# Optimization experiments

Measured on AMD Instinct MI355X. Metric: run time of the kernel, lower is better.

## Reference

```python
import jax, jax.numpy as jnp
import numpy as np

RADIUS = 2          # DKD soft-detection radius -> 5x5 patch
KSIZE = 2 * RADIUS + 1
TEMP = 0.1          # softmax temperature
TOP_K = 2048        # top_k>0 branch: static keypoint count
NMS_R = 3           # simple_nms radius hardcoded in detect_keypoints


def _maxpool(x, r):
    k = 2 * r + 1
    return jax.lax.reduce_window(
        x, -jnp.inf, jax.lax.max,
        (1, 1, k, k), (1, 1, 1, 1),
        ((0, 0), (0, 0), (r, r), (r, r)))


def _maxpool_split(x, r):
    # faithful to max_pool_parallel: pools top/bottom halves independently
    half = x.shape[2] // 2
    return jnp.concatenate([_maxpool(x[:, :, :half], r),
                            _maxpool(x[:, :, half:], r)], axis=2)


def _simple_nms(s, r):
    mm = s == _maxpool_split(s, r)
    for _ in range(2):
        sm = _maxpool_split(mm.astype(s.dtype), r) > 0
        ss = jnp.where(sm, 0.0, s)
        nm = ss == _maxpool_split(ss, r)
        mm = mm | (nm & ~sm)
    return jnp.where(mm, s, 0.0)


def _bilinear(img, xy):
    # grid_sample, mode='bilinear', align_corners=True
    # img: [B,C,H,W], xy: [B,K,2] in [-1,1] (x,y) -> [B,K,C]
    b, c, h, w = img.shape
    imgt = jnp.transpose(img, (0, 2, 3, 1))  # [B,H,W,C]
    x = (xy[..., 0] + 1.0) * 0.5 * (w - 1)
    y = (xy[..., 1] + 1.0) * 0.5 * (h - 1)
    x0 = jnp.floor(x); y0 = jnp.floor(y)
    wx = (x - x0)[..., None]; wy = (y - y0)[..., None]
    x0i = jnp.clip(x0, 0, w - 1).astype(jnp.int32)
    x1i = jnp.clip(x0 + 1, 0, w - 1).astype(jnp.int32)
    y0i = jnp.clip(y0, 0, h - 1).astype(jnp.int32)
    y1i = jnp.clip(y0 + 1, 0, h - 1).astype(jnp.int32)
    bi = jnp.arange(b)[:, None]
    g = lambda yi, xi: imgt[bi, yi, xi]
    return (g(y0i, x0i) * (1 - wx) * (1 - wy) + g(y0i, x1i) * wx * (1 - wy)
            + g(y1i, x0i) * (1 - wx) * wy + g(y1i, x1i) * wx * wy)


def setup_inputs() -> dict:
    key = jax.random.key(0)
    k1, k2 = jax.random.split(key)
    scores_map = jax.random.uniform(k1, (2, 1, 512, 512), dtype=jnp.float32)
    descriptor_map = jax.random.normal(k2, (2, 128, 512, 512), dtype=jnp.float32)
    return {"scores_map": scores_map, "descriptor_map": descriptor_map}


def reference(scores_map, descriptor_map):
    b, _, h, w = scores_map.shape
    r = RADIUS
    dt = scores_map.dtype
    # --- NMS on detached scores ---
    s_ng = jax.lax.stop_gradient(scores_map)
    nms = _simple_nms(s_ng, NMS_R)
    yi = jnp.arange(h); xi = jnp.arange(w)
    border = (((yi >= r + 1) & (yi < h - r))[:, None]
              & ((xi >= r + 1) & (xi < w - r))[None, :])
    nms = nms * border
    # --- top_k keypoint selection (static shape [B,K]) ---
    _, idx = jax.lax.top_k(nms.reshape(b, -1), TOP_K)
    ky = idx // w; kx = idx % w
    # --- gather 5x5 patches (== unfold + fancy index), zero padded ---
    pad = jnp.pad(scores_map[:, 0], ((0, 0), (r, r), (r, r)))
    offs = jnp.arange(KSIZE)
    dyg, dxg = jnp.meshgrid(offs, offs, indexing='ij')
    dy = dyg.reshape(-1); dx = dxg.reshape(-1)           # [25]
    bi = jnp.arange(b)[:, None, None]
    patch = pad[bi, ky[:, :, None] + dy, kx[:, :, None] + dx]   # [B,K,25]
    # hw_grid: (dx, dy) pairs, row-major over (dy, dx) like unfold
    lin = jnp.linspace(-r, r, KSIZE).astype(dt)
    gy, gx = jnp.meshgrid(lin, lin, indexing='ij')
    hw = jnp.stack([gx.reshape(-1), gy.reshape(-1)], axis=-1)   # [25,2]
    # --- soft-argmax subpixel refinement ---
    maxv = jax.lax.stop_gradient(patch.max(-1, keepdims=True))
    xexp = jnp.exp((patch - maxv) / TEMP)
    ssum = xexp.sum(-1)
    xy_res = jnp.einsum('bkp,pc->bkc', xexp, hw) / ssum[..., None]  # [B,K,2]
    d2 = jnp.sum(((hw[None, None] - xy_res[:, :, None]) / r) ** 2, axis=-1)
    disp = (xexp * d2).sum(-1) / ssum                     # [B,K]
    kxy = jnp.stack([kx, ky], axis=-1).astype(dt) + xy_res
    kxy = kxy / jnp.array([w - 1, h - 1], dt) * 2.0 - 1.0  # [-1,1]
    # --- bilinear sampling of scores + descriptors ---
    kptscores = _bilinear(scores_map, kxy)[..., 0]        # [B,K]
    desc = _bilinear(descriptor_map, kxy)                 # [B,K,C]
    desc = desc / jnp.maximum(jnp.linalg.norm(desc, axis=-1, keepdims=True), 1e-12)
    return (kxy, desc, kptscores, disp)
```

## Files before the change

### kernel.cpp

```cpp
#include <hip/hip_runtime.h>
#include <cstdint>
#include <cstddef>

#define H 512
#define W 512
#define NPIX (H * W)
#define TOPK 2048
#define CAND_CAP 4096
#define NBATCH 2

#define RG 62
#define RS 64
#define NTOT (RG * RS)

struct Tap {
    int x0, x1, y0, y1;
    float wx, wy;
    float pad0, pad1;
};

__global__ void k_zero(unsigned int* __restrict__ hist, unsigned int* __restrict__ cnt) {
    int i = blockIdx.x * 256 + threadIdx.x;
    if (i < NBATCH * 65536) hist[i] = 0;
    if (i < 8) cnt[i] = 0;
}

__global__ __launch_bounds__(256) void k_nms_fused(
        const float* __restrict__ s, float* __restrict__ nms,
        unsigned int* __restrict__ hist) {
    __shared__ float A[NTOT];
    __shared__ float Bf[NTOT];
    __shared__ float Cf[NTOT];
    __shared__ unsigned char Mmm[NTOT];
    __shared__ unsigned char Msm[NTOT];
    __shared__ unsigned char Mt[NTOT];

    const int tid = threadIdx.x;
    const int b = blockIdx.z;
    const int gx0 = blockIdx.x * 32 - 15;
    const int gy0 = blockIdx.y * 32 - 15;
    const int h0 = (blockIdx.y < 8) ? 0 : 256;
    const int h1 = h0 + 256;
    const float* sb = s + (size_t)b * NPIX;

    for (int i = tid; i < NTOT; i += 256) {
        int x = i & 63, y = i >> 6;
        float v = -INFINITY;
        int gx = gx0 + x, gy = gy0 + y;
        if (x < RG && gx >= 0 && gx < W && gy >= h0 && gy < h1)
            v = sb[gy * W + gx];
        A[i] = v;
    }
    __syncthreads();

    for (int i = tid; i < NTOT; i += 256) {
        int x = i & 63;
        if (x >= 3 && x < 59) {
            float m = A[i - 3];
            m = fmaxf(m, A[i - 2]); m = fmaxf(m, A[i - 1]); m = fmaxf(m, A[i]);
            m = fmaxf(m, A[i + 1]); m = fmaxf(m, A[i + 2]); m = fmaxf(m, A[i + 3]);
            Cf[i] = m;
        }
    }
    __syncthreads();

    for (int i = tid; i < NTOT; i += 256) {
        int x = i & 63, y = i >> 6;
        if (x >= 3 && x < 59 && y >= 3 && y < 59) {
            float m = Cf[i - 3 * RS];
            m = fmaxf(m, Cf[i - 2 * RS]); m = fmaxf(m, Cf[i - RS]);
            m = fmaxf(m, Cf[i]);
            m = fmaxf(m, Cf[i + RS]); m = fmaxf(m, Cf[i + 2 * RS]);
            m = fmaxf(m, Cf[i + 3 * RS]);
            Mmm[i] = (A[i] == m) ? 1 : 0;
        }
    }
    __syncthreads();

    for (int it = 0; it < 2; ++it) {
        const int lo1 = 6 + 6 * it, hi1 = RG - lo1;
        const int lo0 = lo1 - 3,    hi0 = RG - lo0;
        const int lo2 = lo1 + 3,    hi2 = RG - lo2;

        for (int i = tid; i < NTOT; i += 256) {
            int x = i & 63, y = i >> 6;
            if (x >= lo1 && x < hi1 && y >= lo0 && y < hi0) {
                Mt[i] = (unsigned char)(Mmm[i - 3] | Mmm[i - 2] | Mmm[i - 1] |
                                        Mmm[i] | Mmm[i + 1] | Mmm[i + 2] | Mmm[i + 3]);
            }
        }
        __syncthreads();

        for (int i = tid; i < NTOT; i += 256) {
            int x = i & 63, y = i >> 6;
            if (x >= lo1 && x < hi1 && y >= lo1 && y < hi1) {
                unsigned char o = (unsigned char)(Mt[i - 3 * RS] | Mt[i - 2 * RS] |
                                                  Mt[i - RS] | Mt[i] | Mt[i + RS] |
                                                  Mt[i + 2 * RS] | Mt[i + 3 * RS]);
                Msm[i] = o;
                Bf[i] = o ? 0.0f : A[i];
            }
        }
        __syncthreads();

        for (int i = tid; i < NTOT; i += 256) {
            int x = i & 63, y = i >> 6;
            if (x >= lo2 && x < hi2 && y >= lo1 && y < hi1) {
                float m = Bf[i - 3];
                m = fmaxf(m, Bf[i - 2]); m = fmaxf(m, Bf[i - 1]); m = fmaxf(m, Bf[i]);
                m = fmaxf(m, Bf[i + 1]); m = fmaxf(m, Bf[i + 2]); m = fmaxf(m, Bf[i + 3]);
                Cf[i] = m;
            }
        }
        __syncthreads();

        if (it == 0) {
            for (int i = tid; i < NTOT; i += 256) {
                int x = i & 63, y = i >> 6;
                if (x >= lo2 && x < hi2 && y >= lo2 && y < hi2) {
                    float m = Cf[i - 3 * RS];
                    m = fmaxf(m, Cf[i - 2 * RS]); m = fmaxf(m, Cf[i - RS]);
                    m = fmaxf(m, Cf[i]);
                    m = fmaxf(m, Cf[i + RS]); m = fmaxf(m, Cf[i + 2 * RS]);
                    m = fmaxf(m, Cf[i + 3 * RS]);
                    int nm = (Bf[i] == m) ? 1 : 0;
                    Mmm[i] = (unsigned char)(Mmm[i] | (nm & (1 - (int)Msm[i])));
                }
            }
            __syncthreads();
        } else {
            for (int i = tid; i < NTOT; i += 256) {
                int x = i & 63, y = i >> 6;
                if (x >= 15 && x < 47 && y >= 15 && y < 47) {
                    float m = Cf[i - 3 * RS];
                    m = fmaxf(m, Cf[i - 2 * RS]); m = fmaxf(m, Cf[i - RS]);
                    m = fmaxf(m, Cf[i]);
                    m = fmaxf(m, Cf[i + RS]); m = fmaxf(m, Cf[i + 2 * RS]);
                    m = fmaxf(m, Cf[i + 3 * RS]);
                    int nm = (Bf[i] == m) ? 1 : 0;
                    int mm2 = Mmm[i] | (nm & (1 - (int)Msm[i]));
                    int gx = gx0 + x, gy = gy0 + y;
                    bool border = (gx >= 3) && (gx < 510) && (gy >= 3) && (gy < 510);
                    float v = (mm2 && border) ? A[i] : 0.0f;
                    nms[(size_t)b * NPIX + gy * W + gx] = v;
                    if (v > 0.0f) {
                        unsigned int key = __float_as_uint(v);
                        atomicAdd(&hist[b * 65536 + (key >> 16)], 1u);
                    }
                }
            }
        }
    }
}

__global__ __launch_bounds__(1024) void k_thresh(const unsigned int* __restrict__ hist,
                                                 unsigned int* __restrict__ tb) {
    int b = blockIdx.x;
    const unsigned int* h = hist + b * 65536;
    __shared__ unsigned int scan[1024];
    __shared__ int cstar;
    int t = threadIdx.x;

    unsigned int acc = 0;
    const uint4* h4 = reinterpret_cast<const uint4*>(h + t * 64);
    #pragma unroll
    for (int i = 0; i < 16; ++i) { uint4 v = h4[i]; acc += v.x + v.y + v.z + v.w; }
    scan[t] = acc;
    if (t == 0) cstar = -1;
    __syncthreads();
    for (int d = 1; d < 1024; d <<= 1) {
        unsigned int v = (t + d < 1024) ? scan[t + d] : 0;
        __syncthreads();
        scan[t] += v;
        __syncthreads();
    }
    unsigned int Snext = (t < 1023) ? scan[t + 1] : 0;
    if (scan[t] >= TOPK && (t == 1023 || Snext < TOPK)) cstar = t;
    __syncthreads();
    int c = cstar;
    if (c < 0) {
        if (t == 0) tb[b] = 0;
        return;
    }
    if (t < 64) {
        unsigned int above = (c < 1023) ? scan[c + 1] : 0;
        unsigned int suf = h[c * 64 + t];
        #pragma unroll
        for (int d = 1; d < 64; d <<= 1) {
            unsigned int v2 = __shfl_down(suf, d, 64);
            suf += (t + d < 64) ? v2 : 0;
        }
        bool cond = (above + suf) >= (unsigned int)TOPK;
        unsigned long long msk = __ballot(cond);
        if (t == 0) tb[b] = (unsigned int)(c * 64 + (63 - __clzll(msk)));
    }
}

__global__ void k_collect(const float* __restrict__ nms, const unsigned int* __restrict__ tb,
                          unsigned long long* __restrict__ cand, unsigned int* __restrict__ cnt) {
    int t = blockIdx.x * blockDim.x + threadIdx.x;
    if (t >= NBATCH * NPIX) return;
    float v = nms[t];
    if (v > 0.0f) {
        int b = t >> 18;
        unsigned int key = __float_as_uint(v);
        if ((key >> 16) >= tb[b]) {
            unsigned int pos = atomicAdd(&cnt[b], 1u);
            if (pos < CAND_CAP) {
                unsigned int pix = (unsigned int)(t & (NPIX - 1));
                cand[b * CAND_CAP + pos] =
                    ((unsigned long long)key << 32) | (unsigned long long)(~pix);
            }
        }
    }
}

__global__ __launch_bounds__(256) void k_rank(const unsigned long long* __restrict__ cand,
                                              const unsigned int* __restrict__ cnt,
                                              int* __restrict__ kpts) {
    __shared__ unsigned long long sk[CAND_CAP];
    int b = blockIdx.y;
    int tid = threadIdx.x;
    unsigned int n = cnt[b];
    if (n > CAND_CAP) n = CAND_CAP;
    const unsigned long long* cb = cand + b * CAND_CAP;
    for (int i = tid; i < CAND_CAP; i += 256)
        sk[i] = (i < (int)n) ? cb[i] : 0ULL;
    __syncthreads();
    int i = blockIdx.x * 256 + tid;
    if (i < (int)n) {
        unsigned long long my = sk[i];
        int rank = 0;
        int j = 0;
        int n4 = (int)n & ~3;
        for (; j < n4; j += 4) {
            rank += (sk[j] > my) + (sk[j + 1] > my) + (sk[j + 2] > my) + (sk[j + 3] > my);
        }
        for (; j < (int)n; ++j) rank += (sk[j] > my);
        if (rank < TOPK) {
            unsigned int pix = ~(unsigned int)(my & 0xFFFFFFFFULL);
            kpts[b * TOPK + rank] = (int)pix;
        }
    }
}

__global__ void k_soft(const float* __restrict__ s, const int* __restrict__ kpts,
                       float* __restrict__ out_kxy, float* __restrict__ out_sc,
                       float* __restrict__ out_disp, Tap* __restrict__ taps) {
    int t = blockIdx.x * blockDim.x + threadIdx.x;
    if (t >= NBATCH * TOPK) return;
    int b = t >> 11;
    int pix = kpts[t];
    int ky = (pix >> 9) & 511, kx = pix & 511;
    const float* sb = s + (size_t)b * NPIX;

    float p[25];
    float maxv = -INFINITY;
    #pragma unroll
    for (int i = 0; i < 5; ++i)
        #pragma unroll
        for (int j = 0; j < 5; ++j) {
            float v = sb[(ky - 2 + i) * W + (kx - 2 + j)];
            p[i * 5 + j] = v;
            maxv = fmaxf(maxv, v);
        }
    float e[25];
    float ssum = 0.0f, sx = 0.0f, sy = 0.0f;
    #pragma unroll
    for (int i = 0; i < 5; ++i)
        #pragma unroll
        for (int j = 0; j < 5; ++j) {
            float ev = expf((p[i * 5 + j] - maxv) / 0.1f);
            e[i * 5 + j] = ev;
            ssum += ev;
            sx += ev * (float)(j - 2);
            sy += ev * (float)(i - 2);
        }
    float xr = sx / ssum, yr = sy / ssum;
    float acc = 0.0f;
    #pragma unroll
    for (int i = 0; i < 5; ++i)
        #pragma unroll
        for (int j = 0; j < 5; ++j) {
            float dx = ((float)(j - 2) - xr) * 0.5f;
            float dy = ((float)(i - 2) - yr) * 0.5f;
            acc += e[i * 5 + j] * (dx * dx + dy * dy);
        }
    float disp = acc / ssum;

    float nx = ((float)kx + xr) / 511.0f * 2.0f - 1.0f;
    float ny = ((float)ky + yr) / 511.0f * 2.0f - 1.0f;
    out_kxy[t * 2 + 0] = nx;
    out_kxy[t * 2 + 1] = ny;
    out_disp[t] = disp;

    float xp = (nx + 1.0f) * 0.5f * 511.0f;
    float yp = (ny + 1.0f) * 0.5f * 511.0f;
    float x0 = floorf(xp), y0 = floorf(yp);
    float wxf = xp - x0, wyf = yp - y0;
    int x0i = (int)fminf(fmaxf(x0, 0.0f), 511.0f);
    int x1i = (int)fminf(fmaxf(x0 + 1.0f, 0.0f), 511.0f);
    int y0i = (int)fminf(fmaxf(y0, 0.0f), 511.0f);
    int y1i = (int)fminf(fmaxf(y0 + 1.0f, 0.0f), 511.0f);
    float v00 = sb[y0i * W + x0i], v01 = sb[y0i * W + x1i];
    float v10 = sb[y1i * W + x0i], v11 = sb[y1i * W + x1i];
    out_sc[t] = v00 * (1.0f - wxf) * (1.0f - wyf) + v01 * wxf * (1.0f - wyf)
              + v10 * (1.0f - wxf) * wyf + v11 * wxf * wyf;

    Tap tp;
    tp.x0 = x0i; tp.x1 = x1i; tp.y0 = y0i; tp.y1 = y1i;
    tp.wx = wxf; tp.wy = wyf; tp.pad0 = 0.0f; tp.pad1 = 0.0f;
    taps[t] = tp;
}

__global__ void k_desc(const float* __restrict__ dmap, const Tap* __restrict__ taps,
                       float* __restrict__ out_desc) {
    int t = blockIdx.x;
    int b = t >> 11;
    int c = threadIdx.x;
    Tap tp = taps[t];
    const float* db = dmap + ((size_t)(b * 128 + c)) * NPIX;
    float w00 = (1.0f - tp.wx) * (1.0f - tp.wy);
    float w01 = tp.wx * (1.0f - tp.wy);
    float w10 = (1.0f - tp.wx) * tp.wy;
    float w11 = tp.wx * tp.wy;
    float v = db[tp.y0 * W + tp.x0] * w00 + db[tp.y0 * W + tp.x1] * w01
            + db[tp.y1 * W + tp.x0] * w10 + db[tp.y1 * W + tp.x1] * w11;

    float sq = v * v;
    #pragma unroll
    for (int m = 32; m >= 1; m >>= 1) sq += __shfl_xor(sq, m, 64);
    __shared__ float red[2];
    int wave = c >> 6, lane = c & 63;
    if (lane == 0) red[wave] = sq;
    __syncthreads();
    float tot = red[0] + red[1];
    float nrm = sqrtf(tot);
    float sc = 1.0f / fmaxf(nrm, 1e-12f);
    out_desc[(size_t)t * 128 + c] = v * sc;
}

extern "C" void kernel_launch(void* const* d_in, const int* in_sizes, int n_in,
                              void* d_out, int out_size, void* d_ws, size_t ws_size,
                              hipStream_t stream) {
    const float* s    = (const float*)d_in[0];
    const float* dmap = (const float*)d_in[1];
    float* out = (float*)d_out;
    float* out_kxy  = out;
    float* out_desc = out + 8192;
    float* out_sc   = out + 8192 + 524288;
    float* out_disp = out_sc + 4096;

    char* w = (char*)d_ws;
    float* nms           = (float*)w;          w += (size_t)NBATCH * NPIX * 4;
    unsigned int* hist   = (unsigned int*)w;   w += (size_t)NBATCH * 65536 * 4;
    unsigned long long* cand = (unsigned long long*)w; w += (size_t)NBATCH * CAND_CAP * 8;
    unsigned int* cnt    = (unsigned int*)w;   w += 256;
    unsigned int* tb     = (unsigned int*)w;   w += 256;
    int* kpts            = (int*)w;            w += (size_t)NBATCH * TOPK * 4;
    Tap* taps            = (Tap*)w;            w += (size_t)NBATCH * TOPK * sizeof(Tap);

    k_zero<<<dim3(512), dim3(256), 0, stream>>>(hist, cnt);
    k_nms_fused<<<dim3(16, 16, NBATCH), dim3(256), 0, stream>>>(s, nms, hist);
    k_thresh<<<dim3(NBATCH), dim3(1024), 0, stream>>>(hist, tb);
    k_collect<<<dim3((NBATCH * NPIX) / 256), dim3(256), 0, stream>>>(nms, tb, cand, cnt);
    k_rank<<<dim3(CAND_CAP / 256, NBATCH), dim3(256), 0, stream>>>(cand, cnt, kpts);
    k_soft<<<dim3((NBATCH * TOPK) / 256), dim3(256), 0, stream>>>(s, kpts, out_kxy, out_sc, out_disp, taps);
    k_desc<<<dim3(NBATCH * TOPK), dim3(128), 0, stream>>>(dmap, taps, out_desc);
}
```

Baseline: 509.9 us.

## Emit sparse NMS keypoint list instead of dense map; fuse rank with soft refine

The NMS kernel now appends surviving keypoints to a compact per-batch list and no longer writes a dense 2x512x512 NMS map. The dense collect pass is replaced by a small filter over that list. Rank and soft-argmax refinement are merged into one kernel, and the shared-memory stencil loops now process two pixels per thread using float2 and 16-bit mask accesses. This removes a full-map write and re-read plus a launch, at the cost of a second global atomic per survivor and a list capped at 65536 entries per batch.

```diff
diff --git a/kernel.cpp b/kernel.cpp
--- a/kernel.cpp
+++ b/kernel.cpp
@@ -7,11 +7,13 @@
 #define NPIX (H * W)
 #define TOPK 2048
 #define CAND_CAP 4096
+#define LIST_CAP 65536
 #define NBATCH 2
 
 #define RG 62
 #define RS 64
 #define NTOT (RG * RS)
+#define NPAIR (RG * 32)
 
 struct Tap {
     int x0, x1, y0, y1;
@@ -19,15 +21,20 @@
     float pad0, pad1;
 };
 
-__global__ void k_zero(unsigned int* __restrict__ hist, unsigned int* __restrict__ cnt) {
+#define F2(arr, i) (*reinterpret_cast<float2*>(&(arr)[(i)]))
+#define U16(arr, i) (*reinterpret_cast<unsigned short*>(&(arr)[(i)]))
+
+__global__ void k_zero(unsigned int* __restrict__ hist, unsigned int* __restrict__ cnts) {
     int i = blockIdx.x * 256 + threadIdx.x;
     if (i < NBATCH * 65536) hist[i] = 0;
-    if (i < 8) cnt[i] = 0;
+    if (i < 16) cnts[i] = 0;
 }
 
 __global__ __launch_bounds__(256) void k_nms_fused(
-        const float* __restrict__ s, float* __restrict__ nms,
-        unsigned int* __restrict__ hist) {
+        const float* __restrict__ s,
+        unsigned int* __restrict__ hist,
+        unsigned long long* __restrict__ list,
+        unsigned int* __restrict__ gcnt) {
     __shared__ float A[NTOT];
     __shared__ float Bf[NTOT];
     __shared__ float Cf[NTOT];
@@ -53,27 +60,35 @@
     }
     __syncthreads();
 
-    for (int i = tid; i < NTOT; i += 256) {
-        int x = i & 63;
-        if (x >= 3 && x < 59) {
-            float m = A[i - 3];
-            m = fmaxf(m, A[i - 2]); m = fmaxf(m, A[i - 1]); m = fmaxf(m, A[i]);
-            m = fmaxf(m, A[i + 1]); m = fmaxf(m, A[i + 2]); m = fmaxf(m, A[i + 3]);
-            Cf[i] = m;
-        }
-    }
-    __syncthreads();
-
-    for (int i = tid; i < NTOT; i += 256) {
-        int x = i & 63, y = i >> 6;
-        if (x >= 3 && x < 59 && y >= 3 && y < 59) {
-            float m = Cf[i - 3 * RS];
-            m = fmaxf(m, Cf[i - 2 * RS]); m = fmaxf(m, Cf[i - RS]);
-            m = fmaxf(m, Cf[i]);
-            m = fmaxf(m, Cf[i + RS]); m = fmaxf(m, Cf[i + 2 * RS]);
-            m = fmaxf(m, Cf[i + 3 * RS]);
-            Mmm[i] = (A[i] == m) ? 1 : 0;
-        }
+    for (int pi = tid; pi < NPAIR; pi += 256) {
+        int y = pi >> 5, x = (pi & 31) * 2;
+        if (x < 2 || x > 58) continue;
+        int i = y * RS + x;
+        float2 a0 = F2(A, i - 2), a1 = F2(A, i), a2 = F2(A, i + 2);
+        float c6 = fmaxf(fmaxf(fmaxf(a0.x, a0.y), fmaxf(a1.x, a1.y)), fmaxf(a2.x, a2.y));
+        float lft = (i >= 3) ? A[i - 3] : -INFINITY;
+        float o0 = fmaxf(c6, lft);
+        float o1 = fmaxf(c6, A[i + 4]);
+        if (x >= 3 && x < 59) Cf[i] = o0;
+        if (x + 1 < 59) Cf[i + 1] = o1;
+    }
+    __syncthreads();
+
+    for (int pi = tid; pi < NPAIR; pi += 256) {
+        int y = pi >> 5, x = (pi & 31) * 2;
+        if (y < 3 || y >= 59 || x < 2 || x > 58) continue;
+        int i = y * RS + x;
+        float2 m = F2(Cf, i - 3 * RS);
+        float2 c;
+        c = F2(Cf, i - 2 * RS); m.x = fmaxf(m.x, c.x); m.y = fmaxf(m.y, c.y);
+        c = F2(Cf, i - RS);     m.x = fmaxf(m.x, c.x); m.y = fmaxf(m.y, c.y);
+        c = F2(Cf, i);          m.x = fmaxf(m.x, c.x); m.y = fmaxf(m.y, c.y);
+        c = F2(Cf, i + RS);     m.x = fmaxf(m.x, c.x); m.y = fmaxf(m.y, c.y);
+        c = F2(Cf, i + 2 * RS); m.x = fmaxf(m.x, c.x); m.y = fmaxf(m.y, c.y);
+        c = F2(Cf, i + 3 * RS); m.x = fmaxf(m.x, c.x); m.y = fmaxf(m.y, c.y);
+        float2 a = F2(A, i);
+        if (x >= 3 && x < 59)  Mmm[i] = (a.x == m.x) ? 1 : 0;
+        if (x + 1 < 59)        Mmm[i + 1] = (a.y == m.y) ? 1 : 0;
     }
     __syncthreads();
 
@@ -82,70 +97,110 @@
         const int lo0 = lo1 - 3,    hi0 = RG - lo0;
         const int lo2 = lo1 + 3,    hi2 = RG - lo2;
 
-        for (int i = tid; i < NTOT; i += 256) {
-            int x = i & 63, y = i >> 6;
-            if (x >= lo1 && x < hi1 && y >= lo0 && y < hi0) {
-                Mt[i] = (unsigned char)(Mmm[i - 3] | Mmm[i - 2] | Mmm[i - 1] |
-                                        Mmm[i] | Mmm[i + 1] | Mmm[i + 2] | Mmm[i + 3]);
-            }
+        for (int pi = tid; pi < NPAIR; pi += 256) {
+            int y = pi >> 5, x = (pi & 31) * 2;
+            if (y < lo0 || y >= hi0 || x < lo1 || x >= hi1) continue;
+            int i = y * RS + x;
+            unsigned int u = (unsigned int)U16(Mmm, i - 2) | U16(Mmm, i) | U16(Mmm, i + 2);
+            unsigned int common = (u | (u >> 8)) & 0xFF;
+            unsigned int o0 = common | Mmm[i - 3];
+            unsigned int o1 = common | Mmm[i + 4];
+            U16(Mt, i) = (unsigned short)(o0 | (o1 << 8));
         }
         __syncthreads();
 
-        for (int i = tid; i < NTOT; i += 256) {
-            int x = i & 63, y = i >> 6;
-            if (x >= lo1 && x < hi1 && y >= lo1 && y < hi1) {
-                unsigned char o = (unsigned char)(Mt[i - 3 * RS] | Mt[i - 2 * RS] |
-                                                  Mt[i - RS] | Mt[i] | Mt[i + RS] |
-                                                  Mt[i + 2 * RS] | Mt[i + 3 * RS]);
-                Msm[i] = o;
-                Bf[i] = o ? 0.0f : A[i];
-            }
+        for (int pi = tid; pi < NPAIR; pi += 256) {
+            int y = pi >> 5, x = (pi & 31) * 2;
+            if (y < lo1 || y >= hi1 || x < lo1 || x >= hi1) continue;
+            int i = y * RS + x;
+            unsigned int o = (unsigned int)U16(Mt, i - 3 * RS) | U16(Mt, i - 2 * RS) |
+                             U16(Mt, i - RS) | U16(Mt, i) | U16(Mt, i + RS) |
+                             U16(Mt, i + 2 * RS) | U16(Mt, i + 3 * RS);
+            U16(Msm, i) = (unsigned short)o;
+            float2 a = F2(A, i);
+            float2 bb;
+            bb.x = (o & 0xFF) ? 0.0f : a.x;
+            bb.y = (o >> 8)   ? 0.0f : a.y;
+            F2(Bf, i) = bb;
         }
         __syncthreads();
 
-        for (int i = tid; i < NTOT; i += 256) {
-            int x = i & 63, y = i >> 6;
-            if (x >= lo2 && x < hi2 && y >= lo1 && y < hi1) {
-                float m = Bf[i - 3];
-                m = fmaxf(m, Bf[i - 2]); m = fmaxf(m, Bf[i - 1]); m = fmaxf(m, Bf[i]);
-                m = fmaxf(m, Bf[i + 1]); m = fmaxf(m, Bf[i + 2]); m = fmaxf(m, Bf[i + 3]);
-                Cf[i] = m;
-            }
+        for (int pi = tid; pi < NPAIR; pi += 256) {
+            int y = pi >> 5, x = (pi & 31) * 2;
+            if (y < lo1 || y >= hi1) continue;
+            if (x + 1 < lo2 || x >= hi2) continue;
+            int i = y * RS + x;
+            float2 a0 = F2(Bf, i - 2), a1 = F2(Bf, i), a2 = F2(Bf, i + 2);
+            float c6 = fmaxf(fmaxf(fmaxf(a0.x, a0.y), fmaxf(a1.x, a1.y)), fmaxf(a2.x, a2.y));
+            float o0 = fmaxf(c6, Bf[i - 3]);
+            float o1 = fmaxf(c6, Bf[i + 4]);
+            if (x >= lo2 && x < hi2)     Cf[i] = o0;
+            if (x + 1 >= lo2 && x + 1 < hi2) Cf[i + 1] = o1;
         }
         __syncthreads();
 
         if (it == 0) {
-            for (int i = tid; i < NTOT; i += 256) {
-                int x = i & 63, y = i >> 6;
-                if (x >= lo2 && x < hi2 && y >= lo2 && y < hi2) {
-                    float m = Cf[i - 3 * RS];
-                    m = fmaxf(m, Cf[i - 2 * RS]); m = fmaxf(m, Cf[i - RS]);
-                    m = fmaxf(m, Cf[i]);
-                    m = fmaxf(m, Cf[i + RS]); m = fmaxf(m, Cf[i + 2 * RS]);
-                    m = fmaxf(m, Cf[i + 3 * RS]);
-                    int nm = (Bf[i] == m) ? 1 : 0;
+            for (int pi = tid; pi < NPAIR; pi += 256) {
+                int y = pi >> 5, x = (pi & 31) * 2;
+                if (y < lo2 || y >= hi2) continue;
+                if (x + 1 < lo2 || x >= hi2) continue;
+                int i = y * RS + x;
+                float2 m = F2(Cf, i - 3 * RS);
+                float2 c;
+                c = F2(Cf, i - 2 * RS); m.x = fmaxf(m.x, c.x); m.y = fmaxf(m.y, c.y);
+                c = F2(Cf, i - RS);     m.x = fmaxf(m.x, c.x); m.y = fmaxf(m.y, c.y);
+                c = F2(Cf, i);          m.x = fmaxf(m.x, c.x); m.y = fmaxf(m.y, c.y);
+                c = F2(Cf, i + RS);     m.x = fmaxf(m.x, c.x); m.y = fmaxf(m.y, c.y);
+                c = F2(Cf, i + 2 * RS); m.x = fmaxf(m.x, c.x); m.y = fmaxf(m.y, c.y);
+                c = F2(Cf, i + 3 * RS); m.x = fmaxf(m.x, c.x); m.y = fmaxf(m.y, c.y);
+                float2 bb = F2(Bf, i);
+                if (x >= lo2 && x < hi2) {
+                    int nm = (bb.x == m.x) ? 1 : 0;
                     Mmm[i] = (unsigned char)(Mmm[i] | (nm & (1 - (int)Msm[i])));
+                }
+                if (x + 1 >= lo2 && x + 1 < hi2) {
+                    int nm = (bb.y == m.y) ? 1 : 0;
+                    Mmm[i + 1] = (unsigned char)(Mmm[i + 1] | (nm & (1 - (int)Msm[i + 1])));
                 }
             }
             __syncthreads();
         } else {
-            for (int i = tid; i < NTOT; i += 256) {
-                int x = i & 63, y = i >> 6;
-                if (x >= 15 && x < 47 && y >= 15 && y < 47) {
-                    float m = Cf[i - 3 * RS];
-                    m = fmaxf(m, Cf[i - 2 * RS]); m = fmaxf(m, Cf[i - RS]);
-                    m = fmaxf(m, Cf[i]);
-                    m = fmaxf(m, Cf[i + RS]); m = fmaxf(m, Cf[i + 2 * RS]);
-                    m = fmaxf(m, Cf[i + 3 * RS]);
-                    int nm = (Bf[i] == m) ? 1 : 0;
-                    int mm2 = Mmm[i] | (nm & (1 - (int)Msm[i]));
-                    int gx = gx0 + x, gy = gy0 + y;
+            for (int pi = tid; pi < NPAIR; pi += 256) {
+                int y = pi >> 5, x = (pi & 31) * 2;
+                if (y < 15 || y >= 47) continue;
+                if (x + 1 < 15 || x >= 47) continue;
+                int i = y * RS + x;
+                float2 m = F2(Cf, i - 3 * RS);
+                float2 c;
+                c = F2(Cf, i - 2 * RS); m.x = fmaxf(m.x, c.x); m.y = fmaxf(m.y, c.y);
+                c = F2(Cf, i - RS);     m.x = fmaxf(m.x, c.x); m.y = fmaxf(m.y, c.y);
+                c = F2(Cf, i);          m.x = fmaxf(m.x, c.x); m.y = fmaxf(m.y, c.y);
+                c = F2(Cf, i + RS);     m.x = fmaxf(m.x, c.x); m.y = fmaxf(m.y, c.y);
+                c = F2(Cf, i + 2 * RS); m.x = fmaxf(m.x, c.x); m.y = fmaxf(m.y, c.y);
+                c = F2(Cf, i + 3 * RS); m.x = fmaxf(m.x, c.x); m.y = fmaxf(m.y, c.y);
+                float2 bb = F2(Bf, i);
+                float2 aa = F2(A, i);
+                #pragma unroll
+                for (int e = 0; e < 2; ++e) {
+                    int xe = x + e;
+                    if (xe < 15 || xe >= 47) continue;
+                    float bv = e ? bb.y : bb.x;
+                    float mv = e ? m.y : m.x;
+                    float av = e ? aa.y : aa.x;
+                    int nm = (bv == mv) ? 1 : 0;
+                    int mm2 = Mmm[i + e] | (nm & (1 - (int)Msm[i + e]));
+                    int gx = gx0 + xe, gy = gy0 + y;
                     bool border = (gx >= 3) && (gx < 510) && (gy >= 3) && (gy < 510);
-                    float v = (mm2 && border) ? A[i] : 0.0f;
-                    nms[(size_t)b * NPIX + gy * W + gx] = v;
+                    float v = (mm2 && border) ? av : 0.0f;
                     if (v > 0.0f) {
                         unsigned int key = __float_as_uint(v);
                         atomicAdd(&hist[b * 65536 + (key >> 16)], 1u);
+                        unsigned int pos = atomicAdd(&gcnt[b], 1u);
+                        if (pos < LIST_CAP) {
+                            unsigned int pix = (unsigned int)(gy * W + gx);
+                            list[(size_t)b * LIST_CAP + pos] =
+                                ((unsigned long long)key << 32) | (unsigned long long)(~pix);
+                        }
                     }
                 }
             }
@@ -196,103 +251,94 @@
     }
 }
 
-__global__ void k_collect(const float* __restrict__ nms, const unsigned int* __restrict__ tb,
-                          unsigned long long* __restrict__ cand, unsigned int* __restrict__ cnt) {
-    int t = blockIdx.x * blockDim.x + threadIdx.x;
-    if (t >= NBATCH * NPIX) return;
-    float v = nms[t];
-    if (v > 0.0f) {
-        int b = t >> 18;
-        unsigned int key = __float_as_uint(v);
-        if ((key >> 16) >= tb[b]) {
-            unsigned int pos = atomicAdd(&cnt[b], 1u);
-            if (pos < CAND_CAP) {
-                unsigned int pix = (unsigned int)(t & (NPIX - 1));
-                cand[b * CAND_CAP + pos] =
-                    ((unsigned long long)key << 32) | (unsigned long long)(~pix);
-            }
-        }
-    }
-}
-
-__global__ __launch_bounds__(256) void k_rank(const unsigned long long* __restrict__ cand,
-                                              const unsigned int* __restrict__ cnt,
-                                              int* __restrict__ kpts) {
+__global__ void k_filter(const unsigned long long* __restrict__ list,
+                         const unsigned int* __restrict__ gcnt,
+                         const unsigned int* __restrict__ tb,
+                         unsigned long long* __restrict__ cand,
+                         unsigned int* __restrict__ cnt2) {
+    int i = blockIdx.x * 256 + threadIdx.x;
+    int b = i >> 16;
+    int idx = i & (LIST_CAP - 1);
+    unsigned int n = gcnt[b];
+    if (n > LIST_CAP) n = LIST_CAP;
+    if (idx >= (int)n) return;
+    unsigned long long comp = list[(size_t)b * LIST_CAP + idx];
+    unsigned int key = (unsigned int)(comp >> 32);
+    if ((key >> 16) >= tb[b]) {
+        unsigned int pos = atomicAdd(&cnt2[b], 1u);
+        if (pos < CAND_CAP) cand[b * CAND_CAP + pos] = comp;
+    }
+}
+
+__global__ __launch_bounds__(256) void k_rank_soft(
+        const unsigned long long* __restrict__ cand,
+        const unsigned int* __restrict__ cnt2,
+        const float* __restrict__ s,
+        float* __restrict__ out_kxy, float* __restrict__ out_sc,
+        float* __restrict__ out_disp, Tap* __restrict__ taps) {
     __shared__ unsigned long long sk[CAND_CAP];
     int b = blockIdx.y;
     int tid = threadIdx.x;
-    unsigned int n = cnt[b];
+    unsigned int n = cnt2[b];
     if (n > CAND_CAP) n = CAND_CAP;
     const unsigned long long* cb = cand + b * CAND_CAP;
     for (int i = tid; i < CAND_CAP; i += 256)
         sk[i] = (i < (int)n) ? cb[i] : 0ULL;
     __syncthreads();
     int i = blockIdx.x * 256 + tid;
-    if (i < (int)n) {
-        unsigned long long my = sk[i];
-        int rank = 0;
-        int j = 0;
-        int n4 = (int)n & ~3;
-        for (; j < n4; j += 4) {
-            rank += (sk[j] > my) + (sk[j + 1] > my) + (sk[j + 2] > my) + (sk[j + 3] > my);
-        }
-        for (; j < (int)n; ++j) rank += (sk[j] > my);
-        if (rank < TOPK) {
-            unsigned int pix = ~(unsigned int)(my & 0xFFFFFFFFULL);
-            kpts[b * TOPK + rank] = (int)pix;
-        }
-    }
-}
-
-__global__ void k_soft(const float* __restrict__ s, const int* __restrict__ kpts,
-                       float* __restrict__ out_kxy, float* __restrict__ out_sc,
-                       float* __restrict__ out_disp, Tap* __restrict__ taps) {
-    int t = blockIdx.x * blockDim.x + threadIdx.x;
-    if (t >= NBATCH * TOPK) return;
-    int b = t >> 11;
-    int pix = kpts[t];
-    int ky = (pix >> 9) & 511, kx = pix & 511;
+    if (i >= (int)n) return;
+    unsigned long long my = sk[i];
+    int rank = 0;
+    int j = 0;
+    int n4 = (int)n & ~3;
+    for (; j < n4; j += 4)
+        rank += (sk[j] > my) + (sk[j + 1] > my) + (sk[j + 2] > my) + (sk[j + 3] > my);
+    for (; j < (int)n; ++j) rank += (sk[j] > my);
+    if (rank >= TOPK) return;
+
+    int t = b * TOPK + rank;
+    unsigned int pix = ~(unsigned int)(my & 0xFFFFFFFFULL);
+    int ky = (int)(pix >> 9) & 511, kx = (int)pix & 511;
     const float* sb = s + (size_t)b * NPIX;
 
     float p[25];
     float maxv = -INFINITY;
     #pragma unroll
-    for (int i = 0; i < 5; ++i)
+    for (int ii = 0; ii < 5; ++ii)
         #pragma unroll
-        for (int j = 0; j < 5; ++j) {
-            float v = sb[(ky - 2 + i) * W + (kx - 2 + j)];
-            p[i * 5 + j] = v;
+        for (int jj = 0; jj < 5; ++jj) {
+            float v = sb[(ky - 2 + ii) * W + (kx - 2 + jj)];
+            p[ii * 5 + jj] = v;
             maxv = fmaxf(maxv, v);
         }
     float e[25];
     float ssum = 0.0f, sx = 0.0f, sy = 0.0f;
     #pragma unroll
-    for (int i = 0; i < 5; ++i)
+    for (int ii = 0; ii < 5; ++ii)
         #pragma unroll
-        for (int j = 0; j < 5; ++j) {
-            float ev = expf((p[i * 5 + j] - maxv) / 0.1f);
-            e[i * 5 + j] = ev;
+        for (int jj = 0; jj < 5; ++jj) {
+            float ev = expf((p[ii * 5 + jj] - maxv) / 0.1f);
+            e[ii * 5 + jj] = ev;
             ssum += ev;
-            sx += ev * (float)(j - 2);
-            sy += ev * (float)(i - 2);
+            sx += ev * (float)(jj - 2);
+            sy += ev * (float)(ii - 2);
         }
     float xr = sx / ssum, yr = sy / ssum;
     float acc = 0.0f;
     #pragma unroll
-    for (int i = 0; i < 5; ++i)
+    for (int ii = 0; ii < 5; ++ii)
         #pragma unroll
-        for (int j = 0; j < 5; ++j) {
-            float dx = ((float)(j - 2) - xr) * 0.5f;
-            float dy = ((float)(i - 2) - yr) * 0.5f;
-            acc += e[i * 5 + j] * (dx * dx + dy * dy);
-        }
-    float disp = acc / ssum;
+        for (int jj = 0; jj < 5; ++jj) {
+            float dx = ((float)(jj - 2) - xr) * 0.5f;
+            float dy = ((float)(ii - 2) - yr) * 0.5f;
+            acc += e[ii * 5 + jj] * (dx * dx + dy * dy);
+        }
+    out_disp[t] = acc / ssum;
 
     float nx = ((float)kx + xr) / 511.0f * 2.0f - 1.0f;
     float ny = ((float)ky + yr) / 511.0f * 2.0f - 1.0f;
-    out_kxy[t * 2 + 0] = nx;
-    out_kxy[t * 2 + 1] = ny;
-    out_disp[t] = disp;
+    float2 kxy; kxy.x = nx; kxy.y = ny;
+    *reinterpret_cast<float2*>(&out_kxy[t * 2]) = kxy;
 
     float xp = (nx + 1.0f) * 0.5f * 511.0f;
     float yp = (ny + 1.0f) * 0.5f * 511.0f;
@@ -352,19 +398,19 @@
     float* out_disp = out_sc + 4096;
 
     char* w = (char*)d_ws;
-    float* nms           = (float*)w;          w += (size_t)NBATCH * NPIX * 4;
-    unsigned int* hist   = (unsigned int*)w;   w += (size_t)NBATCH * 65536 * 4;
+    unsigned int* hist       = (unsigned int*)w;       w += (size_t)NBATCH * 65536 * 4;
+    unsigned long long* list = (unsigned long long*)w; w += (size_t)NBATCH * LIST_CAP * 8;
     unsigned long long* cand = (unsigned long long*)w; w += (size_t)NBATCH * CAND_CAP * 8;
-    unsigned int* cnt    = (unsigned int*)w;   w += 256;
-    unsigned int* tb     = (unsigned int*)w;   w += 256;
-    int* kpts            = (int*)w;            w += (size_t)NBATCH * TOPK * 4;
-    Tap* taps            = (Tap*)w;            w += (size_t)NBATCH * TOPK * sizeof(Tap);
-
-    k_zero<<<dim3(512), dim3(256), 0, stream>>>(hist, cnt);
-    k_nms_fused<<<dim3(16, 16, NBATCH), dim3(256), 0, stream>>>(s, nms, hist);
+    unsigned int* cnts       = (unsigned int*)w;       w += 256;
+    unsigned int* tb         = (unsigned int*)w;       w += 256;
+    Tap* taps                = (Tap*)w;                w += (size_t)NBATCH * TOPK * sizeof(Tap);
+    unsigned int* gcnt = cnts;
+    unsigned int* cnt2 = cnts + 2;
+
+    k_zero<<<dim3(512), dim3(256), 0, stream>>>(hist, cnts);
+    k_nms_fused<<<dim3(16, 16, NBATCH), dim3(256), 0, stream>>>(s, hist, list, gcnt);
     k_thresh<<<dim3(NBATCH), dim3(1024), 0, stream>>>(hist, tb);
-    k_collect<<<dim3((NBATCH * NPIX) / 256), dim3(256), 0, stream>>>(nms, tb, cand, cnt);
-    k_rank<<<dim3(CAND_CAP / 256, NBATCH), dim3(256), 0, stream>>>(cand, cnt, kpts);
-    k_soft<<<dim3((NBATCH * TOPK) / 256), dim3(256), 0, stream>>>(s, kpts, out_kxy, out_sc, out_disp, taps);
+    k_filter<<<dim3((NBATCH * LIST_CAP) / 256), dim3(256), 0, stream>>>(list, gcnt, tb, cand, cnt2);
+    k_rank_soft<<<dim3(CAND_CAP / 256, NBATCH), dim3(256), 0, stream>>>(cand, cnt2, s, out_kxy, out_sc, out_disp, taps);
     k_desc<<<dim3(NBATCH * TOPK), dim3(128), 0, stream>>>(dmap, taps, out_desc);
 }
```

Result: slower. 581.7 us (+14.1%).
